# Kernel optimization log

Hardware: AMD Instinct MI355X
Metric: run time of the kernel (lower is better)

The kernel has to match this reference:

```python
import jax, jax.numpy as jnp
import numpy as np

NUM_TILES = 64
TPC = 8            # tiles per cluster
GRID = 16          # spline grid size
EPS = 1e-5


def setup_inputs() -> dict:
    key = jax.random.key(0)
    ks = jax.random.split(key, 6)
    B, S, D, T, DH, G = 2, 1024, 512, NUM_TILES, 128, GRID
    x = jax.random.normal(ks[0], (B, S, D), dtype=jnp.float32)
    gamma = jnp.ones((D,), jnp.float32)
    beta = jnp.zeros((D,), jnp.float32)
    # torch layouts: down.weight [DH, D], up.weight [D, DH]
    Wd = jax.random.normal(ks[1], (T, DH, D), dtype=jnp.float32) * 0.02
    spline_bases = jax.random.normal(ks[2], (T, DH, G), dtype=jnp.float32) * 0.1
    spline_slopes = jax.random.normal(ks[3], (T, DH, G), dtype=jnp.float32) * 0.1
    Wu = jax.random.normal(ks[4], (T, D, DH), dtype=jnp.float32) * 0.02
    scale = jnp.full((T,), 0.1, jnp.float32)
    return {"x": x, "gamma": gamma, "beta": beta, "Wd": Wd,
            "spline_bases": spline_bases, "spline_slopes": spline_slopes,
            "Wu": Wu, "scale": scale}


def reference(x, gamma, beta, Wd, spline_bases, spline_slopes, Wu, scale):
    B, S, D = x.shape
    T, DH, _ = Wd.shape
    C = T // TPC
    N = B * S

    # LayerNorm
    mu = x.mean(-1, keepdims=True)
    var = ((x - mu) ** 2).mean(-1, keepdims=True)
    xn = (x - mu) * jax.lax.rsqrt(var + EPS) * gamma + beta
    xf = xn.reshape(N, D)

    # Signatures (first call: ema == current tile signatures)
    tile_sigs = jnp.sign(Wd.mean(axis=1))                         # [T, D]
    cluster_sigs = jnp.sign(tile_sigs.reshape(C, TPC, D).mean(1))  # [C, D]

    # Hierarchical routing: cluster -> tile
    in_sigs = jnp.sign(xf)                                        # [N, D]
    best_c = jnp.argmax(in_sigs @ cluster_sigs.T, axis=-1)        # [N]
    tile_scores = (in_sigs @ tile_sigs.T).reshape(N, C, TPC)      # [N, C, TPC]
    sc = jnp.take_along_axis(tile_scores, best_c[:, None, None], axis=1)[:, 0, :]
    local_best = jnp.argmax(sc, axis=-1)                          # [N]
    tidx = best_c * TPC + local_best                              # [N]

    # Dispatch: gather per-token expert weights, down-project
    h = jnp.einsum('nd,nhd->nh', xf, Wd[tidx])                    # [N, DH]

    # Spline nonlinearity
    hn = jax.nn.sigmoid(h)
    idx = jnp.clip((hn * GRID).astype(jnp.int32), 0, GRID - 1)    # [N, DH]
    base = jnp.take_along_axis(spline_bases[tidx], idx[..., None], axis=-1)[..., 0]
    slope = jnp.take_along_axis(spline_slopes[tidx], idx[..., None], axis=-1)[..., 0]
    local_pos = hn * GRID - idx.astype(h.dtype)                   # (hn - idx*cell)/cell
    hs = base + slope * local_pos                                 # [N, DH]

    # Up-project, per-tile scale, combine (dropout is identity in eval)
    y = jnp.einsum('nh,ndh->nd', hs, Wu[tidx]) * scale[tidx][:, None]
    return x + y.reshape(B, S, D)
```

## Files before the change

kernel.cpp:

```cpp
#include <hip/hip_runtime.h>
#include <hip/hip_bf16.h>
#include <math.h>

#define NTILES 64
#define TPC 8
#define NCLUST 8
#define GRID_SZ 16
#define DIM 512
#define DHID 128
#define NTOK 2048
#define LN_EPS 1e-5f
#define TB 16
#define NCHUNK_MAX 192

typedef __attribute__((ext_vector_type(8))) short bf16x8;
typedef __attribute__((ext_vector_type(4))) unsigned short u16x4;
typedef __attribute__((ext_vector_type(4))) float f32x4;
typedef unsigned long long u64;

static __device__ __forceinline__ unsigned short bf16bits(float f) {
    union { __hip_bfloat16 h; unsigned short s; } u;
    u.h = __float2bfloat16(f);
    return u.s;
}

static __device__ __forceinline__ bf16x8 cvt8(const float* p) {
    float4 a = *(const float4*)p;
    float4 b = *(const float4*)(p + 4);
    float e[8] = {a.x, a.y, a.z, a.w, b.x, b.y, b.z, b.w};
    bf16x8 v;
    #pragma unroll
    for (int i = 0; i < 8; ++i) v[i] = (short)bf16bits(e[i]);
    return v;
}

static __device__ __forceinline__ u64 maj3(u64 a, u64 b, u64 c) {
    return (a & b) | (c & (a ^ b));
}

static __device__ __forceinline__ bool route_chunk(const int* counts, int lane, int cb,
                                                   int& t, int& base, int& m) {
    int cnt_l = counts[lane];
    int nck = (cnt_l + TB - 1) / TB;
    int pre = nck;
    #pragma unroll
    for (int off = 1; off < 64; off <<= 1) {
        int u = __shfl_up(pre, off);
        if (lane >= off) pre += u;
    }
    int total = __shfl(pre, 63);
    pre -= nck;
    if (cb >= total) return false;
    u64 msk = __ballot(cb >= pre && cb < pre + nck);
    t = (int)__builtin_ctzll(msk);
    base = (cb - __shfl(pre, t)) * TB;
    m = min(TB, __shfl(cnt_l, t) - base);
    return true;
}

__global__ __launch_bounds__(512) void k_prep(const float* __restrict__ x,
                                              const float* __restrict__ gamma,
                                              const float* __restrict__ beta,
                                              const float* __restrict__ Wd,
                                              const float* __restrict__ Wu,
                                              unsigned short* __restrict__ wd_b,
                                              unsigned short* __restrict__ wu_b,
                                              unsigned short* __restrict__ xn_b,
                                              u64* __restrict__ tbits,
                                              int* __restrict__ counts) {
    int bid = blockIdx.x;
    int tid = threadIdx.x;
    int lane = tid & 63;
    int wv = tid >> 6;
    if (bid < NTILES) {
        int t = bid;
        if (bid == 0 && tid < NTILES) counts[tid] = 0;
        int q = tid >> 7;
        int c4 = tid & 127;
        const float* wp = Wd + ((size_t)t * DHID + q * 32) * DIM + c4 * 4;
        unsigned short* bp = wd_b + ((size_t)t * DHID + q * 32) * DIM + c4 * 4;
        float4 a = {0.f, 0.f, 0.f, 0.f};
        #pragma unroll
        for (int j = 0; j < 32; ++j) {
            float4 v = *(const float4*)(wp + (size_t)j * DIM);
            u16x4 h = {bf16bits(v.x), bf16bits(v.y), bf16bits(v.z), bf16bits(v.w)};
            *(u16x4*)(bp + (size_t)j * DIM) = h;
            a.x += v.x; a.y += v.y; a.z += v.z; a.w += v.w;
        }
        __shared__ float ps[4][DIM];
        *(float4*)&ps[q][c4 * 4] = a;
        __syncthreads();
        float s = ps[0][tid] + ps[1][tid] + ps[2][tid] + ps[3][tid];
        u64 b = __ballot(s < 0.f);
        if (lane == 0) tbits[t * 8 + wv] = b;
    } else if (bid < 320) {
        int n = (bid - NTILES) * 8 + wv;
        const float* xr = x + (size_t)n * DIM;
        float v[8];
        float sum = 0.f;
        #pragma unroll
        for (int j = 0; j < 8; ++j) { float t = xr[lane + 64 * j]; v[j] = t; sum += t; }
        #pragma unroll
        for (int off = 32; off; off >>= 1) sum += __shfl_xor(sum, off);
        float mu = sum * (1.f / DIM);
        float sq = 0.f;
        #pragma unroll
        for (int j = 0; j < 8; ++j) { float t = v[j] - mu; sq += t * t; }
        #pragma unroll
        for (int off = 32; off; off >>= 1) sq += __shfl_xor(sq, off);
        float rs = rsqrtf(sq * (1.f / DIM) + LN_EPS);
        #pragma unroll
        for (int j = 0; j < 8; ++j) {
            int d = lane + 64 * j;
            float xv = (v[j] - mu) * rs * gamma[d] + beta[d];
            xn_b[(size_t)n * DIM + d] = bf16bits(xv);
        }
    } else {
        size_t basei = (size_t)(bid - 320) * 16384;
        #pragma unroll
        for (int k = 0; k < 4; ++k) {
            size_t off = basei + (size_t)tid * 8 + (size_t)k * 4096;
            *(bf16x8*)(wu_b + off) = cvt8(Wu + off);
        }
    }
}

__global__ __launch_bounds__(256) void k_route(const unsigned short* __restrict__ xn_b,
                                               const u64* __restrict__ tbits,
                                               int* __restrict__ counts,
                                               int* __restrict__ list) {
    int n = blockIdx.x * 4 + (threadIdx.x >> 6);
    int lane = threadIdx.x & 63;
    u64 xb[8];
    #pragma unroll
    for (int j = 0; j < 8; ++j) {
        unsigned short u = xn_b[(size_t)n * DIM + lane + 64 * j];
        xb[j] = __ballot((u & 0x8000u) != 0 && (u & 0x7fffu) != 0);
    }
    const u64* tb = tbits + lane * 8;
    int ts = 0;
    #pragma unroll
    for (int j = 0; j < 8; ++j) ts += __popcll(xb[j] ^ tb[j]);
    int tscore = DIM - 2 * ts;

    int c = lane >> 3, jw = lane & 7;
    u64 x0 = tbits[(c * TPC + 0) * 8 + jw], x1 = tbits[(c * TPC + 1) * 8 + jw];
    u64 x2 = tbits[(c * TPC + 2) * 8 + jw], x3 = tbits[(c * TPC + 3) * 8 + jw];
    u64 x4 = tbits[(c * TPC + 4) * 8 + jw], x5 = tbits[(c * TPC + 5) * 8 + jw];
    u64 x6 = tbits[(c * TPC + 6) * 8 + jw], x7 = tbits[(c * TPC + 7) * 8 + jw];
    u64 s0 = x0 ^ x1 ^ x2, c0 = maj3(x0, x1, x2);
    u64 s1 = x3 ^ x4 ^ x5, c1 = maj3(x3, x4, x5);
    u64 s2 = x6 ^ x7,      c2 = x6 & x7;
    u64 t0 = s0 ^ s1 ^ s2, t1 = maj3(s0, s1, s2);
    u64 p = c0 ^ c1, q = c0 & c1;
    u64 r = c2 ^ t1, s_ = c2 & t1;
    u64 S0 = p ^ r, car = p & r;
    u64 W0 = (q ^ s_) ^ car;
    u64 W1 = (q & s_) | (car & (q ^ s_));
    u64 cbit = W1 | (W0 & (S0 | t0));
    u64 cmsk = ~(W0 & ~W1 & ~S0 & ~t0);
    int psc = __popcll(cmsk) - 2 * __popcll((xb[jw] ^ cbit) & cmsk);
    psc += __shfl_xor(psc, 1);
    psc += __shfl_xor(psc, 2);
    psc += __shfl_xor(psc, 4);

    int bc = 0, best = __shfl(psc, 0);
    #pragma unroll
    for (int k = 1; k < NCLUST; ++k) {
        int v = __shfl(psc, k * 8);
        if (v > best) { best = v; bc = k; }
    }
    int bt = bc * TPC, bts = __shfl(tscore, bc * TPC);
    #pragma unroll
    for (int k = 1; k < TPC; ++k) {
        int v = __shfl(tscore, bc * TPC + k);
        if (v > bts) { bts = v; bt = bc * TPC + k; }
    }
    if (lane == 0) {
        int slot = atomicAdd(&counts[bt], 1);
        list[(size_t)bt * NTOK + slot] = n;
    }
}

__global__ __launch_bounds__(512, 1) void k_ffn(const float* __restrict__ x,
                                                const unsigned short* __restrict__ xn_b,
                                                const unsigned short* __restrict__ wd_b,
                                                const float* __restrict__ sb,
                                                const float* __restrict__ ss,
                                                const unsigned short* __restrict__ wu_b,
                                                const float* __restrict__ scale,
                                                const int* __restrict__ counts,
                                                const int* __restrict__ list,
                                                float* __restrict__ out) {
    int tid = threadIdx.x;
    int lane = tid & 63;
    int wv = tid >> 6;
    int cb = ((int)blockIdx.x & 7) * (NCHUNK_MAX / 8) + ((int)blockIdx.x >> 3);
    int t, base, m;
    if (!route_chunk(counts, lane, cb, t, base, m)) return;

    __shared__ __align__(16) unsigned short hsl[TB * DHID];

    int mrow = lane & 15;
    int ko = (lane >> 4) * 8;
    int tokm = list[(size_t)t * NTOK + base + min(mrow, m - 1)];

    const unsigned short* xr = xn_b + (size_t)tokm * DIM;
    const unsigned short* wr = wd_b + ((size_t)t * DHID + wv * 16 + mrow) * DIM;
    bf16x8 wreg[16], areg[16];
    #pragma unroll
    for (int kk = 0; kk < 16; ++kk) {
        int d = kk * 32 + ko;
        wreg[kk] = *(const bf16x8*)(wr + d);
        areg[kk] = *(const bf16x8*)(xr + d);
    }
    f32x4 acc0 = {0.f, 0.f, 0.f, 0.f}, acc1 = acc0;
    #pragma unroll
    for (int kk = 0; kk < 8; ++kk) {
        acc0 = __builtin_amdgcn_mfma_f32_16x16x32_bf16(areg[2 * kk], wreg[2 * kk], acc0, 0, 0, 0);
        acc1 = __builtin_amdgcn_mfma_f32_16x16x32_bf16(areg[2 * kk + 1], wreg[2 * kk + 1], acc1, 0, 0, 0);
    }
    f32x4 acc = acc0 + acc1;

    bf16x8 wupf[16];
    #pragma unroll
    for (int nt = 0; nt < 4; ++nt) {
        const unsigned short* wru = wu_b + ((size_t)t * DIM + wv * 64 + nt * 16 + mrow) * DHID;
        #pragma unroll
        for (int kk = 0; kk < 4; ++kk)
            wupf[nt * 4 + kk] = *(const bf16x8*)(wru + kk * 32 + ko);
    }

    int tokr[4];
    #pragma unroll
    for (int r = 0; r < 4; ++r) tokr[r] = __shfl(tokm, (lane >> 4) * 4 + r);
    float xpf[4][4];
    #pragma unroll
    for (int r = 0; r < 4; ++r) {
        #pragma unroll
        for (int nt = 0; nt < 4; ++nt)
            xpf[r][nt] = x[(size_t)tokr[r] * DIM + wv * 64 + nt * 16 + mrow];
    }

    int dh = wv * 16 + mrow;
    const float* sbt = sb + ((size_t)t * DHID + dh) * GRID_SZ;
    const float* sst = ss + ((size_t)t * DHID + dh) * GRID_SZ;
    #pragma unroll
    for (int r = 0; r < 4; ++r) {
        int tr = (lane >> 4) * 4 + r;
        float h = acc[r];
        float hn = 1.f / (1.f + expf(-h));
        float g = hn * (float)GRID_SZ;
        int idx = (int)g;
        idx = idx > GRID_SZ - 1 ? GRID_SZ - 1 : idx;
        float lp = g - (float)idx;
        float val = sbt[idx] + sst[idx] * lp;
        hsl[(tr * DHID + dh) ^ ((tr & 7) << 3)] = bf16bits(val);
    }
    __syncthreads();

    float sc_t = scale[t];
    bf16x8 a2[4];
    #pragma unroll
    for (int kk = 0; kk < 4; ++kk)
        a2[kk] = *(const bf16x8*)&hsl[(mrow * DHID + kk * 32 + ko) ^ ((mrow & 7) << 3)];
    #pragma unroll
    for (int nt = 0; nt < 4; ++nt) {
        int d = wv * 64 + nt * 16 + mrow;
        f32x4 au = {0.f, 0.f, 0.f, 0.f};
        #pragma unroll
        for (int kk = 0; kk < 4; ++kk)
            au = __builtin_amdgcn_mfma_f32_16x16x32_bf16(a2[kk], wupf[nt * 4 + kk], au, 0, 0, 0);
        #pragma unroll
        for (int r = 0; r < 4; ++r) {
            int tr = (lane >> 4) * 4 + r;
            if (tr < m) {
                size_t o = (size_t)tokr[r] * DIM + d;
                out[o] = xpf[r][nt] + au[r] * sc_t;
            }
        }
    }
}

extern "C" void kernel_launch(void* const* d_in, const int* in_sizes, int n_in,
                              void* d_out, int out_size, void* d_ws, size_t ws_size,
                              hipStream_t stream) {
    const float* x     = (const float*)d_in[0];
    const float* gamma = (const float*)d_in[1];
    const float* beta  = (const float*)d_in[2];
    const float* Wd    = (const float*)d_in[3];
    const float* sb    = (const float*)d_in[4];
    const float* ss    = (const float*)d_in[5];
    const float* Wu    = (const float*)d_in[6];
    const float* scale = (const float*)d_in[7];
    float* out = (float*)d_out;

    u64*   tbits         = (u64*)d_ws;
    int*   counts        = (int*)(tbits + NTILES * 8);
    int*   list          = counts + NTILES;
    unsigned short* xn_b = (unsigned short*)(list + (size_t)NTILES * NTOK);
    unsigned short* wd_b = xn_b + (size_t)NTOK * DIM;
    unsigned short* wu_b = wd_b + (size_t)NTILES * DHID * DIM;

    k_prep<<<576, 512, 0, stream>>>(x, gamma, beta, Wd, Wu, wd_b, wu_b, xn_b, tbits, counts);
    k_route<<<NTOK / 4, 256, 0, stream>>>(xn_b, tbits, counts, list);
    k_ffn<<<NCHUNK_MAX, 512, 0, stream>>>(x, xn_b, wd_b, sb, ss, wu_b, scale, counts, list, out);
}
```

Baseline: 43.18 us.

## Split Wd conversion across four blocks per tile with last-block sign reduction

The Wd bf16 conversion and column-sum work per tile is spread over four blocks instead of one. Each block writes a partial column sum to a workspace buffer, and the last block to finish, found with an atomic counter, combines the partials and emits the sign bits. Each thread also issues all eight row loads up front for more memory-level parallelism. The cost is an added hipMemsetAsync, atomics and fences, and a larger grid for the prep kernel.

```diff
diff --git a/kernel.cpp b/kernel.cpp
--- a/kernel.cpp
+++ b/kernel.cpp
@@ -66,35 +66,52 @@
                                               unsigned short* __restrict__ wd_b,
                                               unsigned short* __restrict__ wu_b,
                                               unsigned short* __restrict__ xn_b,
+                                              float* __restrict__ psum,
                                               u64* __restrict__ tbits,
-                                              int* __restrict__ counts) {
+                                              int* __restrict__ prog) {
     int bid = blockIdx.x;
     int tid = threadIdx.x;
     int lane = tid & 63;
     int wv = tid >> 6;
-    if (bid < NTILES) {
-        int t = bid;
-        if (bid == 0 && tid < NTILES) counts[tid] = 0;
-        int q = tid >> 7;
+    if (bid < 256) {
+        int t = bid >> 2, q = bid & 3;
+        int r0 = tid >> 7;
         int c4 = tid & 127;
-        const float* wp = Wd + ((size_t)t * DHID + q * 32) * DIM + c4 * 4;
-        unsigned short* bp = wd_b + ((size_t)t * DHID + q * 32) * DIM + c4 * 4;
+        const float* wp = Wd + ((size_t)t * DHID + q * 32 + r0 * 8) * DIM + c4 * 4;
+        unsigned short* bp = wd_b + ((size_t)t * DHID + q * 32 + r0 * 8) * DIM + c4 * 4;
+        float4 v[8];
+        #pragma unroll
+        for (int k = 0; k < 8; ++k) v[k] = *(const float4*)(wp + (size_t)k * DIM);
         float4 a = {0.f, 0.f, 0.f, 0.f};
         #pragma unroll
-        for (int j = 0; j < 32; ++j) {
-            float4 v = *(const float4*)(wp + (size_t)j * DIM);
-            u16x4 h = {bf16bits(v.x), bf16bits(v.y), bf16bits(v.z), bf16bits(v.w)};
-            *(u16x4*)(bp + (size_t)j * DIM) = h;
-            a.x += v.x; a.y += v.y; a.z += v.z; a.w += v.w;
+        for (int k = 0; k < 8; ++k) {
+            u16x4 h = {bf16bits(v[k].x), bf16bits(v[k].y), bf16bits(v[k].z), bf16bits(v[k].w)};
+            *(u16x4*)(bp + (size_t)k * DIM) = h;
+            a.x += v[k].x; a.y += v[k].y; a.z += v[k].z; a.w += v[k].w;
         }
         __shared__ float ps[4][DIM];
-        *(float4*)&ps[q][c4 * 4] = a;
+        __shared__ int lastf;
+        *(float4*)&ps[r0][c4 * 4] = a;
         __syncthreads();
         float s = ps[0][tid] + ps[1][tid] + ps[2][tid] + ps[3][tid];
-        u64 b = __ballot(s < 0.f);
-        if (lane == 0) tbits[t * 8 + wv] = b;
-    } else if (bid < 320) {
-        int n = (bid - NTILES) * 8 + wv;
+        psum[(size_t)(t * 4 + q) * DIM + tid] = s;
+        __syncthreads();
+        if (tid == 0) {
+            __threadfence();
+            lastf = (atomicAdd(&prog[t], 1) == 3);
+        }
+        __syncthreads();
+        if (lastf) {
+            __threadfence();
+            float sum = psum[(size_t)(t * 4 + 0) * DIM + tid]
+                      + psum[(size_t)(t * 4 + 1) * DIM + tid]
+                      + psum[(size_t)(t * 4 + 2) * DIM + tid]
+                      + psum[(size_t)(t * 4 + 3) * DIM + tid];
+            u64 b = __ballot(sum < 0.f);
+            if (lane == 0) tbits[t * 8 + wv] = b;
+        }
+    } else if (bid < 512) {
+        int n = (bid - 256) * 8 + wv;
         const float* xr = x + (size_t)n * DIM;
         float v[8];
         float sum = 0.f;
@@ -116,7 +133,7 @@
             xn_b[(size_t)n * DIM + d] = bf16bits(xv);
         }
     } else {
-        size_t basei = (size_t)(bid - 320) * 16384;
+        size_t basei = (size_t)(bid - 512) * 16384;
         #pragma unroll
         for (int k = 0; k < 4; ++k) {
             size_t off = basei + (size_t)tid * 8 + (size_t)k * 4096;
@@ -295,14 +312,17 @@
     const float* scale = (const float*)d_in[7];
     float* out = (float*)d_out;
 
-    u64*   tbits         = (u64*)d_ws;
-    int*   counts        = (int*)(tbits + NTILES * 8);
-    int*   list          = counts + NTILES;
-    unsigned short* xn_b = (unsigned short*)(list + (size_t)NTILES * NTOK);
+    int*   prog          = (int*)d_ws;
+    int*   counts        = prog + NTILES;
+    u64*   tbits         = (u64*)(counts + NTILES);
+    int*   list          = (int*)(tbits + NTILES * 8);
+    float* psum          = (float*)(list + (size_t)NTILES * NTOK);
+    unsigned short* xn_b = (unsigned short*)(psum + 256 * DIM);
     unsigned short* wd_b = xn_b + (size_t)NTOK * DIM;
     unsigned short* wu_b = wd_b + (size_t)NTILES * DHID * DIM;
 
-    k_prep<<<576, 512, 0, stream>>>(x, gamma, beta, Wd, Wu, wd_b, wu_b, xn_b, tbits, counts);
+    hipMemsetAsync(prog, 0, 512, stream);
+    k_prep<<<768, 512, 0, stream>>>(x, gamma, beta, Wd, Wu, wd_b, wu_b, xn_b, psum, tbits, prog);
     k_route<<<NTOK / 4, 256, 0, stream>>>(xn_b, tbits, counts, list);
     k_ffn<<<NCHUNK_MAX, 512, 0, stream>>>(x, xn_b, wd_b, sb, ss, wu_b, scale, counts, list, out);
 }
```

Result: slower. 88.25 us (+104.4%).
